# Optimization experiments

Measured on AMD Instinct MI355X. Metric: run time of the kernel, lower is better.

The kernel has to match this reference:

```python
import jax, jax.numpy as jnp
import numpy as np

MARGIN = 0.3
W_HUMAN = 1.0
W_PER = 1.0
NUM_CLASSES = 16
EPS = 1e-8


def setup_inputs() -> dict:
    key = jax.random.key(0)
    k1, k2, k3, k4, k5, k6 = jax.random.split(key, 6)
    B, D, T = 4096, 1024, 100000
    return {
        "preds_mat": jax.random.normal(k1, (B, NUM_CLASSES), dtype=jnp.float32),
        "preds_sub": jax.random.normal(k2, (B, 4), dtype=jnp.float32),
        "inputs": jax.random.normal(k3, (B, D), dtype=jnp.float32),
        "targets_mat": jax.random.randint(k4, (B,), 0, NUM_CLASSES, dtype=jnp.int64),
        "targets_sub": jax.random.randint(k5, (B,), 0, 4, dtype=jnp.int64),
        "user_answers": jax.random.randint(k6, (T, 3), 0, NUM_CLASSES, dtype=jnp.int64),
    }


def _pairwise_dist(x):
    # Euclidean pairwise distance: [B, B]
    sq = jnp.sum(x * x, axis=1)
    d2 = sq[:, None] + sq[None, :] - 2.0 * (x @ x.T)
    return jnp.sqrt(jnp.clip(d2, 1e-12))


def reference(preds_mat, preds_sub, inputs, targets_mat, targets_sub, user_answers):
    # Non-classification branch of TripletLossHuman.forward (is_classification=False, unit_norm=False).
    dist = _pairwise_dist(inputs)  # [B, B]

    # which of the NUM_CLASSES material labels are present in this batch
    present = jnp.zeros((NUM_CLASSES,), dtype=bool).at[targets_mat].set(True)
    # a human triplet (anchor,pos,neg labels) is usable iff all 3 labels are present
    valid = jnp.all(present[user_answers], axis=1)  # [T]

    # first occurrence index of each class label in targets_mat (matches torch nonzero()[0])
    first_idx = jnp.argmax(targets_mat[None, :] == jnp.arange(NUM_CLASSES)[:, None], axis=1)  # [C]

    ia = first_idx[user_answers[:, 0]]
    ip = first_idx[user_answers[:, 1]]
    ineg = first_idx[user_answers[:, 2]]
    dist_ap = dist[ia, ip]   # [T]
    dist_an = dist[ia, ineg]  # [T]

    n_valid = jnp.maximum(jnp.sum(valid.astype(dist.dtype)), 1.0)

    # MarginRankingLoss with y=-1: max(0, dist_ap - dist_an + margin), mean over valid triplets
    rank = jnp.maximum(dist_ap - dist_an + MARGIN, 0.0)
    loss_human = jnp.sum(jnp.where(valid, rank, 0.0)) / n_valid

    # perplexity loss
    s_ap = 1.0 / (dist_ap + 1.0)
    s_an = 1.0 / (dist_an + 1.0)
    p_ap = s_ap / (s_ap + s_an)
    per = -jnp.log(p_ap + EPS)
    loss_perplexity = jnp.sum(jnp.where(valid, per, 0.0)) / n_valid

    loss = W_HUMAN * loss_human + W_PER * loss_perplexity
    return jnp.stack([loss, loss_human, loss_perplexity])
```

## Files before the change

### kernel.cpp

```cpp
#include <hip/hip_runtime.h>
#include <math.h>

#define NUM_CLASSES 16
#define MARGIN_F 0.3f
#define EPS_F 1e-8f


__global__ __launch_bounds__(256) void k_dist(const float* __restrict__ x, int Dm,
                                              const int* __restrict__ targets, int B,
                                              float* __restrict__ D16,
                                              float* __restrict__ wsPres,
                                              float* __restrict__ wsAcc,
                                              int* __restrict__ wsCnt) {
    __shared__ int   fi[NUM_CLASSES];
    __shared__ float red[4][3];
    int t = threadIdx.x;
    if (t < NUM_CLASSES) fi[t] = 0x7fffffff;
    __syncthreads();

    int lane = t & 63;
    int waveBase = t & ~63;
    int myMin = 0x7fffffff;
    for (int base = waveBase; base < B; base += 256) {
        int v = (base + lane < B) ? targets[base + lane] : -1;
        #pragma unroll
        for (int c = 0; c < NUM_CLASSES; ++c) {
            unsigned long long m = __ballot(v == c);
            if (lane == c && m != 0ULL) {
                int cand = base + (__ffsll((long long)m) - 1);
                myMin = min(myMin, cand);
            }
        }
    }
    if (lane < NUM_CLASSES && myMin != 0x7fffffff) atomicMin(&fi[lane], myMin);
    __syncthreads();

    if (blockIdx.x == 0) {
        if (t < NUM_CLASSES) wsPres[t] = (fi[t] != 0x7fffffff) ? 1.0f : 0.0f;
        if (t >= 32 && t < 35) wsAcc[t - 32] = 0.0f;
        if (t == 35) *wsCnt = 0;
    }

    int pair = blockIdx.x;
    int c1 = pair >> 4, c2 = pair & 15;
    int i1 = fi[c1], i2 = fi[c2];
    if (i1 == 0x7fffffff) i1 = 0;
    if (i2 == 0x7fffffff) i2 = 0;
    const float4* __restrict__ x1 = (const float4*)(x + (long)i1 * Dm);
    const float4* __restrict__ x2 = (const float4*)(x + (long)i2 * Dm);
    int n4 = Dm >> 2;
    float dot = 0.f, s1 = 0.f, s2 = 0.f;
    for (int k = t; k < n4; k += 256) {
        float4 a = x1[k], b = x2[k];
        dot = fmaf(a.x, b.x, fmaf(a.y, b.y, fmaf(a.z, b.z, fmaf(a.w, b.w, dot))));
        s1  = fmaf(a.x, a.x, fmaf(a.y, a.y, fmaf(a.z, a.z, fmaf(a.w, a.w, s1))));
        s2  = fmaf(b.x, b.x, fmaf(b.y, b.y, fmaf(b.z, b.z, fmaf(b.w, b.w, s2))));
    }
    #pragma unroll
    for (int off = 32; off > 0; off >>= 1) {
        dot += __shfl_down(dot, off);
        s1  += __shfl_down(s1, off);
        s2  += __shfl_down(s2, off);
    }
    int wave = t >> 6;
    if (lane == 0) { red[wave][0] = dot; red[wave][1] = s1; red[wave][2] = s2; }
    __syncthreads();
    if (t == 0) {
        float D = 0.f, A = 0.f, Bq = 0.f;
        #pragma unroll
        for (int w = 0; w < 4; ++w) { D += red[w][0]; A += red[w][1]; Bq += red[w][2]; }
        float d2 = A + Bq - 2.0f * D;
        D16[pair] = sqrtf(fmaxf(d2, 1e-12f));
    }
}

__global__ __launch_bounds__(256) void kB(const int* __restrict__ ua, int T,
                                          const float* __restrict__ D16,
                                          const float* __restrict__ wsPres,
                                          float* __restrict__ wsAcc,
                                          int* __restrict__ wsCnt,
                                          float* __restrict__ out) {
    __shared__ float sD[256];
    __shared__ float sP[NUM_CLASSES];
    __shared__ float sRed[4][3];
    __shared__ bool  amLast;
    int t = threadIdx.x;
    sD[t] = D16[t];
    if (t < NUM_CLASSES) sP[t] = wsPres[t];
    __syncthreads();

    float r = 0.f, pp = 0.f, cnt = 0.f;
    for (int i = blockIdx.x * blockDim.x + t; i < T; i += gridDim.x * blockDim.x) {
        int a = ua[3 * i + 0];
        int b = ua[3 * i + 1];
        int c = ua[3 * i + 2];
        float valid = sP[a] * sP[b] * sP[c];
        float dap = sD[(a << 4) | b];
        float dan = sD[(a << 4) | c];
        float rank = fmaxf(dap - dan + MARGIN_F, 0.0f);
        float sap = 1.0f / (dap + 1.0f);
        float san = 1.0f / (dan + 1.0f);
        float per = -logf(sap / (sap + san) + EPS_F);
        r   += valid * rank;
        pp  += valid * per;
        cnt += valid;
    }
    #pragma unroll
    for (int off = 32; off > 0; off >>= 1) {
        r   += __shfl_down(r, off);
        pp  += __shfl_down(pp, off);
        cnt += __shfl_down(cnt, off);
    }
    int wave = t >> 6, lane = t & 63;
    if (lane == 0) { sRed[wave][0] = r; sRed[wave][1] = pp; sRed[wave][2] = cnt; }
    __syncthreads();
    if (t == 0) {
        float R = 0.f, P = 0.f, C = 0.f;
        #pragma unroll
        for (int w = 0; w < 4; ++w) { R += sRed[w][0]; P += sRed[w][1]; C += sRed[w][2]; }
        atomicAdd(&wsAcc[0], R);
        atomicAdd(&wsAcc[1], P);
        atomicAdd(&wsAcc[2], C);
        __threadfence();
        int done = atomicAdd(wsCnt, 1);
        amLast = (done == (int)gridDim.x - 1);
    }
    __syncthreads();
    if (amLast && t == 0) {
        float R  = atomicAdd(&wsAcc[0], 0.0f);
        float P  = atomicAdd(&wsAcc[1], 0.0f);
        float C  = atomicAdd(&wsAcc[2], 0.0f);
        float nv = fmaxf(C, 1.0f);
        float lh = R / nv;
        float lp = P / nv;
        out[0] = lh + lp;
        out[1] = lh;
        out[2] = lp;
    }
}

extern "C" void kernel_launch(void* const* d_in, const int* in_sizes, int n_in,
                              void* d_out, int out_size, void* d_ws, size_t ws_size,
                              hipStream_t stream) {
    const float* x       = (const float*)d_in[2];
    const int*   targets = (const int*)d_in[3];
    const int*   ua      = (const int*)d_in[5];
    float* out = (float*)d_out;

    int B  = in_sizes[3];
    int Dm = in_sizes[2] / B;
    int T  = in_sizes[5] / 3;

    float* ws     = (float*)d_ws;
    float* D16    = ws;
    float* wsPres = ws + 256;
    float* wsAcc  = ws + 272;
    int*   wsCnt  = (int*)(ws + 275);

    k_dist<<<256, 256, 0, stream>>>(x, Dm, targets, B, D16, wsPres, wsAcc, wsCnt);
    kB<<<256, 256, 0, stream>>>(ua, T, D16, wsPres, wsAcc, wsCnt, out);
}
```

Baseline: 99.77 us.

## Fuse distance and triplet-loss kernels with in-kernel grid barrier

Merges the class-pair distance kernel and the triplet reduction kernel into one launch. A hand-rolled grid barrier (atomic counter plus ready flag with spin-sleep) replaces the kernel boundary. Presence flags are computed in shared memory instead of being written to the workspace. This removes a launch and its gap, but it relies on all 256 blocks being co-resident and on a ready flag that is never cleared between calls, which can race with the counter reset.

```diff
diff --git a/kernel.cpp b/kernel.cpp
--- a/kernel.cpp
+++ b/kernel.cpp
@@ -4,22 +4,40 @@
 #define NUM_CLASSES 16
 #define MARGIN_F 0.3f
 #define EPS_F 1e-8f
+#define READY_MAGIC 0x13579BDF
 
 
-__global__ __launch_bounds__(256) void k_dist(const float* __restrict__ x, int Dm,
-                                              const int* __restrict__ targets, int B,
-                                              float* __restrict__ D16,
-                                              float* __restrict__ wsPres,
-                                              float* __restrict__ wsAcc,
-                                              int* __restrict__ wsCnt) {
+__global__ __launch_bounds__(256) void k_fused(const float* __restrict__ x, int Dm,
+                                               const int* __restrict__ targets, int B,
+                                               const int* __restrict__ ua, int T,
+                                               float* __restrict__ D16,
+                                               float* __restrict__ acc,
+                                               int* __restrict__ cnt1,
+                                               int* __restrict__ cnt2,
+                                               int* __restrict__ ready,
+                                               float* __restrict__ out) {
     __shared__ int   fi[NUM_CLASSES];
     __shared__ float red[4][3];
-    int t = threadIdx.x;
+    __shared__ float sD[256];
+    __shared__ float sP[NUM_CLASSES];
+
+    const int t   = threadIdx.x;
+    const int bid = blockIdx.x;
+
+    if (bid == 0 && t == 0) {
+        __hip_atomic_store(&acc[0], 0.0f, __ATOMIC_RELAXED, __HIP_MEMORY_SCOPE_AGENT);
+        __hip_atomic_store(&acc[1], 0.0f, __ATOMIC_RELAXED, __HIP_MEMORY_SCOPE_AGENT);
+        __hip_atomic_store(&acc[2], 0.0f, __ATOMIC_RELAXED, __HIP_MEMORY_SCOPE_AGENT);
+        __hip_atomic_store(cnt1, 0, __ATOMIC_RELAXED, __HIP_MEMORY_SCOPE_AGENT);
+        __hip_atomic_store(cnt2, 0, __ATOMIC_RELAXED, __HIP_MEMORY_SCOPE_AGENT);
+        __hip_atomic_store(ready, READY_MAGIC, __ATOMIC_RELEASE, __HIP_MEMORY_SCOPE_AGENT);
+    }
+
     if (t < NUM_CLASSES) fi[t] = 0x7fffffff;
     __syncthreads();
 
-    int lane = t & 63;
-    int waveBase = t & ~63;
+    const int lane     = t & 63;
+    const int waveBase = t & ~63;
     int myMin = 0x7fffffff;
     for (int base = waveBase; base < B; base += 256) {
         int v = (base + lane < B) ? targets[base + lane] : -1;
@@ -35,20 +53,13 @@
     if (lane < NUM_CLASSES && myMin != 0x7fffffff) atomicMin(&fi[lane], myMin);
     __syncthreads();
 
-    if (blockIdx.x == 0) {
-        if (t < NUM_CLASSES) wsPres[t] = (fi[t] != 0x7fffffff) ? 1.0f : 0.0f;
-        if (t >= 32 && t < 35) wsAcc[t - 32] = 0.0f;
-        if (t == 35) *wsCnt = 0;
-    }
-
-    int pair = blockIdx.x;
-    int c1 = pair >> 4, c2 = pair & 15;
-    int i1 = fi[c1], i2 = fi[c2];
+    const int pair = bid;
+    int i1 = fi[pair >> 4], i2 = fi[pair & 15];
     if (i1 == 0x7fffffff) i1 = 0;
     if (i2 == 0x7fffffff) i2 = 0;
     const float4* __restrict__ x1 = (const float4*)(x + (long)i1 * Dm);
     const float4* __restrict__ x2 = (const float4*)(x + (long)i2 * Dm);
-    int n4 = Dm >> 2;
+    const int n4 = Dm >> 2;
     float dot = 0.f, s1 = 0.f, s2 = 0.f;
     for (int k = t; k < n4; k += 256) {
         float4 a = x1[k], b = x2[k];
@@ -62,35 +73,31 @@
         s1  += __shfl_down(s1, off);
         s2  += __shfl_down(s2, off);
     }
-    int wave = t >> 6;
+    const int wave = t >> 6;
     if (lane == 0) { red[wave][0] = dot; red[wave][1] = s1; red[wave][2] = s2; }
     __syncthreads();
+
     if (t == 0) {
-        float D = 0.f, A = 0.f, Bq = 0.f;
+        float Dd = 0.f, A = 0.f, Bq = 0.f;
         #pragma unroll
-        for (int w = 0; w < 4; ++w) { D += red[w][0]; A += red[w][1]; Bq += red[w][2]; }
-        float d2 = A + Bq - 2.0f * D;
-        D16[pair] = sqrtf(fmaxf(d2, 1e-12f));
+        for (int w = 0; w < 4; ++w) { Dd += red[w][0]; A += red[w][1]; Bq += red[w][2]; }
+        float d2 = A + Bq - 2.0f * Dd;
+        float d  = sqrtf(fmaxf(d2, 1e-12f));
+        __hip_atomic_store(&D16[pair], d, __ATOMIC_RELAXED, __HIP_MEMORY_SCOPE_AGENT);
+        while (__hip_atomic_load(ready, __ATOMIC_ACQUIRE, __HIP_MEMORY_SCOPE_AGENT) != READY_MAGIC)
+            __builtin_amdgcn_s_sleep(1);
+        __hip_atomic_fetch_add(cnt1, 1, __ATOMIC_ACQ_REL, __HIP_MEMORY_SCOPE_AGENT);
+        while (__hip_atomic_load(cnt1, __ATOMIC_ACQUIRE, __HIP_MEMORY_SCOPE_AGENT) < 256)
+            __builtin_amdgcn_s_sleep(1);
     }
-}
-
-__global__ __launch_bounds__(256) void kB(const int* __restrict__ ua, int T,
-                                          const float* __restrict__ D16,
-                                          const float* __restrict__ wsPres,
-                                          float* __restrict__ wsAcc,
-                                          int* __restrict__ wsCnt,
-                                          float* __restrict__ out) {
-    __shared__ float sD[256];
-    __shared__ float sP[NUM_CLASSES];
-    __shared__ float sRed[4][3];
-    __shared__ bool  amLast;
-    int t = threadIdx.x;
-    sD[t] = D16[t];
-    if (t < NUM_CLASSES) sP[t] = wsPres[t];
     __syncthreads();
 
-    float r = 0.f, pp = 0.f, cnt = 0.f;
-    for (int i = blockIdx.x * blockDim.x + t; i < T; i += gridDim.x * blockDim.x) {
+    sD[t] = __hip_atomic_load(&D16[t], __ATOMIC_RELAXED, __HIP_MEMORY_SCOPE_AGENT);
+    if (t < NUM_CLASSES) sP[t] = (fi[t] != 0x7fffffff) ? 1.0f : 0.0f;
+    __syncthreads();
+
+    float r = 0.f, pp = 0.f, cntv = 0.f;
+    for (int i = bid * 256 + t; i < T; i += 256 * 256) {
         int a = ua[3 * i + 0];
         int b = ua[3 * i + 1];
         int c = ua[3 * i + 2];
@@ -101,41 +108,39 @@
         float sap = 1.0f / (dap + 1.0f);
         float san = 1.0f / (dan + 1.0f);
         float per = -logf(sap / (sap + san) + EPS_F);
-        r   += valid * rank;
-        pp  += valid * per;
-        cnt += valid;
+        r    += valid * rank;
+        pp   += valid * per;
+        cntv += valid;
     }
     #pragma unroll
     for (int off = 32; off > 0; off >>= 1) {
-        r   += __shfl_down(r, off);
-        pp  += __shfl_down(pp, off);
-        cnt += __shfl_down(cnt, off);
+        r    += __shfl_down(r, off);
+        pp   += __shfl_down(pp, off);
+        cntv += __shfl_down(cntv, off);
     }
-    int wave = t >> 6, lane = t & 63;
-    if (lane == 0) { sRed[wave][0] = r; sRed[wave][1] = pp; sRed[wave][2] = cnt; }
+    if (lane == 0) { red[wave][0] = r; red[wave][1] = pp; red[wave][2] = cntv; }
     __syncthreads();
+
     if (t == 0) {
         float R = 0.f, P = 0.f, C = 0.f;
         #pragma unroll
-        for (int w = 0; w < 4; ++w) { R += sRed[w][0]; P += sRed[w][1]; C += sRed[w][2]; }
-        atomicAdd(&wsAcc[0], R);
-        atomicAdd(&wsAcc[1], P);
-        atomicAdd(&wsAcc[2], C);
+        for (int w = 0; w < 4; ++w) { R += red[w][0]; P += red[w][1]; C += red[w][2]; }
+        atomicAdd(&acc[0], R);
+        atomicAdd(&acc[1], P);
+        atomicAdd(&acc[2], C);
         __threadfence();
-        int done = atomicAdd(wsCnt, 1);
-        amLast = (done == (int)gridDim.x - 1);
-    }
-    __syncthreads();
-    if (amLast && t == 0) {
-        float R  = atomicAdd(&wsAcc[0], 0.0f);
-        float P  = atomicAdd(&wsAcc[1], 0.0f);
-        float C  = atomicAdd(&wsAcc[2], 0.0f);
-        float nv = fmaxf(C, 1.0f);
-        float lh = R / nv;
-        float lp = P / nv;
-        out[0] = lh + lp;
-        out[1] = lh;
-        out[2] = lp;
+        int done = atomicAdd(cnt2, 1);
+        if (done == 255) {
+            float Rs = __hip_atomic_load(&acc[0], __ATOMIC_RELAXED, __HIP_MEMORY_SCOPE_AGENT);
+            float Ps = __hip_atomic_load(&acc[1], __ATOMIC_RELAXED, __HIP_MEMORY_SCOPE_AGENT);
+            float Cs = __hip_atomic_load(&acc[2], __ATOMIC_RELAXED, __HIP_MEMORY_SCOPE_AGENT);
+            float nv = fmaxf(Cs, 1.0f);
+            float lh = Rs / nv;
+            float lp = Ps / nv;
+            out[0] = lh + lp;
+            out[1] = lh;
+            out[2] = lp;
+        }
     }
 }
 
@@ -151,12 +156,13 @@
     int Dm = in_sizes[2] / B;
     int T  = in_sizes[5] / 3;
 
-    float* ws     = (float*)d_ws;
-    float* D16    = ws;
-    float* wsPres = ws + 256;
-    float* wsAcc  = ws + 272;
-    int*   wsCnt  = (int*)(ws + 275);
+    float* ws    = (float*)d_ws;
+    float* D16   = ws;
+    float* acc   = ws + 256;
+    int*   cnt1  = (int*)(ws + 259);
+    int*   cnt2  = (int*)(ws + 260);
+    int*   ready = (int*)(ws + 261);
 
-    k_dist<<<256, 256, 0, stream>>>(x, Dm, targets, B, D16, wsPres, wsAcc, wsCnt);
-    kB<<<256, 256, 0, stream>>>(ua, T, D16, wsPres, wsAcc, wsCnt, out);
+    k_fused<<<256, 256, 0, stream>>>(x, Dm, targets, B, ua, T,
+                                     D16, acc, cnt1, cnt2, ready, out);
 }
```

Measured after the change: 107.8 us. 8.1% more time.
